# Kernel optimization log

Hardware: AMD Instinct MI355X
Metric: run time of the kernel (lower is better)

## Reference

```python
import jax, jax.numpy as jnp
import numpy as np

N_E = 1024
E_DIM = 256
BETA = 0.25


def setup_inputs() -> dict:
    key = jax.random.key(0)
    k1, k2 = jax.random.split(key)
    z = jax.random.normal(k1, (32, 256, 32, 32), dtype=jnp.float32)
    # codebook init matches nn.Embedding.weight.data.uniform_(-1/n_e, 1/n_e)
    weight = jax.random.uniform(k2, (N_E, E_DIM), minval=-1.0 / N_E, maxval=1.0 / N_E, dtype=jnp.float32)
    return {"z": z, "weight": weight}


def reference(z, weight):
    B, C, H, W = z.shape  # C == E_DIM
    zp = jnp.transpose(z, (0, 2, 3, 1))          # (B,H,W,C)
    zf = zp.reshape(-1, C)                        # (N, e_dim)
    # squared-distance to every codebook entry: ||z||^2 + ||e||^2 - 2 z.e
    d = (jnp.sum(zf * zf, axis=1, keepdims=True)
         + jnp.sum(weight * weight, axis=1)
         - 2.0 * zf @ weight.T)                   # (N, n_e)
    idx = jnp.argmin(d, axis=1)                   # (N,)
    # one-hot @ weight == direct gather (same math, no dense one-hot)
    z_q = weight[idx].reshape(zp.shape)           # (B,H,W,C)
    loss = (jnp.mean((jax.lax.stop_gradient(z_q) - zp) ** 2)
            + BETA * jnp.mean((z_q - jax.lax.stop_gradient(zp)) ** 2))
    # straight-through estimator
    z_q_st = zp + jax.lax.stop_gradient(z_q - zp)
    # codebook usage (mean of one-hot encodings) -> perplexity
    counts = jnp.zeros((N_E,), jnp.float32).at[idx].add(1.0)
    e_mean = counts / zf.shape[0]
    perplexity = jnp.exp(-jnp.sum(e_mean * jnp.log(e_mean + 1e-10)))
    z_q_out = jnp.transpose(z_q_st, (0, 3, 1, 2))  # (B,C,H,W)
    encoding_indices = idx.reshape(B, H, W)
    return (loss, z_q_out, perplexity, encoding_indices)
```

## Files before the change

### kernel.cpp

```cpp
#include <hip/hip_runtime.h>
#include <math.h>

#define ZQ_ELEMS 8388608
#define ZQ_OFF 1
#define PPLX_OFF (1 + ZQ_ELEMS)
#define IDX_OFF  (2 + ZQ_ELEMS)

typedef __attribute__((ext_vector_type(8))) short short8;
typedef __attribute__((ext_vector_type(4))) float f32x4;
typedef __attribute__((ext_vector_type(16))) float f32x16;

#define WS_CANDC 8192
#define WS_FLAG  139264
#define WS_LIST  270336
#define WS_W2    1843200
#define WS_EBF   1847296

static __device__ __forceinline__ ushort f2bf(float f) {
    uint u = __float_as_uint(f);
    return (ushort)((u + 0x7fffu + ((u >> 16) & 1u)) >> 16);
}

__global__ __launch_bounds__(256) void vq_zero(uint* ws) {
    for (int i = blockIdx.x * 256 + threadIdx.x; i < 67584; i += 64 * 256) ws[i] = 0u;
}

__global__ __launch_bounds__(64) void vq_prep_w2(const float* __restrict__ w,
                                                 float* __restrict__ w2) {
    const int j = blockIdx.x * 64 + threadIdx.x;
    const float* wr = w + (size_t)j * 256;
    float s = 0.f;
    for (int k4 = 0; k4 < 64; ++k4) {
        float4 v = *(const float4*)(wr + k4 * 4);
        s = fmaf(v.x, v.x, s); s = fmaf(v.y, v.y, s);
        s = fmaf(v.z, v.z, s); s = fmaf(v.w, v.w, s);
    }
    w2[j] = s;
}

__global__ __launch_bounds__(256) void vq_prep_e(const float* __restrict__ w,
                                                 ushort* __restrict__ ebf_l) {
    const int g = blockIdx.x * 256 + threadIdx.x;
    const int j = g >> 5, o = g & 31;
    const float* src = w + (size_t)j * 256 + o * 8;
    float4 v0 = *(const float4*)src;
    float4 v1 = *(const float4*)(src + 4);
    short8 r;
    r[0] = (short)f2bf(v0.x); r[1] = (short)f2bf(v0.y);
    r[2] = (short)f2bf(v0.z); r[3] = (short)f2bf(v0.w);
    r[4] = (short)f2bf(v1.x); r[5] = (short)f2bf(v1.y);
    r[6] = (short)f2bf(v1.z); r[7] = (short)f2bf(v1.w);
    const size_t dst = (size_t)(j >> 5) * 8192 + (size_t)(o >> 1) * 512
                     + (size_t)((j & 31) + (o & 1) * 32) * 8;
    *(short8*)(ebf_l + dst) = r;
}

__global__ __launch_bounds__(256) void vq_sweep(const float* __restrict__ z,
                                                const ushort* __restrict__ ebf_l,
                                                const float* __restrict__ w2,
                                                uint* __restrict__ candc,
                                                uint* __restrict__ safeflag,
                                                ushort* __restrict__ lists) {
    __shared__ ushort lcl[128][16];
    __shared__ uint lcnt[128];
    __shared__ float sTr[128];

    const int t = threadIdx.x, wv = t >> 6, l = t & 63;
    const int jq = blockIdx.x & 3, rb = blockIdx.x >> 2;
    const int n0 = rb * 128 + wv * 32;
    const int b = n0 >> 10, hw0 = n0 & 1023;
    const int lj = l & 31, hi = l >> 5;

    for (int i = t; i < 128; i += 256) lcnt[i] = 0u;

    const float* zb = z + (size_t)b * 262144 + hw0 + lj;
    short8 as[16];
    float z2p = 0.f;
    #pragma unroll
    for (int s = 0; s < 16; ++s) {
        short8 fr;
        #pragma unroll
        for (int i = 0; i < 8; ++i) {
            const int k = s * 16 + hi * 8 + i;
            float f = zb[(size_t)k << 10];
            z2p = fmaf(f, f, z2p);
            fr[i] = (short)f2bf(f);
        }
        as[s] = fr;
    }
    z2p += __shfl_xor(z2p, 32);
    if (hi == 0) sTr[wv * 32 + lj] = -2.617e-3f * sqrtf(z2p);
    __syncthreads();

    int rloc[16];
    float TrW[16];
    #pragma unroll
    for (int q = 0; q < 16; ++q) {
        rloc[q] = wv * 32 + (q & 3) + 8 * (q >> 2) + 4 * hi;
        TrW[q] = sTr[rloc[q]];
    }

    const int jbase = jq * 256;
    float w2v[8];
    #pragma unroll
    for (int g = 0; g < 8; ++g) w2v[g] = w2[jbase + g * 32 + lj];

    uint safem = 0u;
    for (int g = 0; g < 8; ++g) {
        const ushort* bt = ebf_l + (size_t)(jq * 8 + g) * 8192;
        f32x16 acc = {};
        #pragma unroll
        for (int s = 0; s < 16; ++s) {
            short8 bf = *(const short8*)(bt + s * 512 + l * 8);
            acc = __builtin_amdgcn_mfma_f32_32x32x16_bf16(as[s], bf, acc, 0, 0, 0);
        }
        const int j = jbase + g * 32 + lj;
        float sv[16];
        bool anyhit = false;
        #pragma unroll
        for (int q = 0; q < 16; ++q) {
            sv[q] = fmaf(-2.f, acc[q], w2v[g]);
            anyhit = anyhit || (sv[q] <= TrW[q]);
        }
        if (__any(anyhit)) {
            #pragma unroll
            for (int q = 0; q < 16; ++q)
                if (sv[q] <= TrW[q]) {
                    uint pos = atomicAdd(&lcnt[rloc[q]], 1u);
                    if (pos < 16u) lcl[rloc[q]][pos] = (ushort)j;
                    if (sv[q] <= TrW[q] - 1.5e-3f) safem |= (1u << q);
                }
        }
    }

    #pragma unroll
    for (int off = 1; off < 32; off <<= 1) safem |= __shfl_xor(safem, off);
    if (lj == 0) {
        #pragma unroll
        for (int q = 0; q < 16; ++q)
            if (safem & (1u << q)) safeflag[rb * 128 + rloc[q]] = 1u;
    }
    __syncthreads();

    if (t < 128) {
        const uint lc = lcnt[t];
        const int n = rb * 128 + t;
        if (lc > 16u) atomicAdd(&candc[n], 100u);
        else if (lc) {
            uint base = atomicAdd(&candc[n], lc);
            for (uint i = 0; i < lc && base + i < 24u; ++i)
                lists[(size_t)n * 24 + base + i] = lcl[t][i];
        }
    }
}

__global__ __launch_bounds__(256) void vq_refine(const float* __restrict__ z,
                                                 const float* __restrict__ w,
                                                 const float* __restrict__ w2,
                                                 const uint* __restrict__ candc,
                                                 const uint* __restrict__ safeflag,
                                                 const ushort* __restrict__ lists,
                                                 float* __restrict__ out,
                                                 float* __restrict__ ws) {
    __shared__ float tile[256][64];
    __shared__ float sz2[64];
    __shared__ int sjmin[64];
    __shared__ int scnt[64];
    __shared__ int soff[65];
    __shared__ uint swl[1536];
    __shared__ float sd[1536];
    __shared__ unsigned long long sfbm;
    __shared__ unsigned long long sred[4];
    __shared__ float lred[4];

    const int t = threadIdx.x;
    const int n0 = blockIdx.x * 64;
    const int b = n0 >> 10, hw0 = n0 & 1023;

    if (t == 0) sfbm = 0ull;

    {
        const int r4 = t & 15, cb = t >> 4;
        for (int i = 0; i < 16; ++i) {
            const int c = i * 16 + cb;
            float4 v = *(const float4*)(z + ((size_t)(b * 256 + c) << 10) + hw0 + r4 * 4);
            *(float4*)&tile[c][r4 * 4] = v;
        }
    }
    __syncthreads();

    if (t < 64) {
        float s = 0.f;
        for (int k = 0; k < 256; ++k) { float v = tile[k][t]; s = fmaf(v, v, s); }
        sz2[t] = s;
    }
    if (t < 64) {
        const int n = n0 + t;
        uint c = candc[n];
        bool fb = (safeflag[n] == 0u) || (c == 0u) || (c > 24u);
        scnt[t] = fb ? 0 : (int)c;
        if (fb) atomicOr(&sfbm, 1ull << t);
    }
    __syncthreads();
    if (t == 0) {
        int acc = 0;
        for (int r = 0; r < 64; ++r) { soff[r] = acc; acc += scnt[r]; }
        soff[64] = acc;
    }
    __syncthreads();
    if (t < 64) {
        const int o = soff[t], c = scnt[t], n = n0 + t;
        for (int i = 0; i < c; ++i) swl[o + i] = ((uint)t << 16) | (uint)lists[(size_t)n * 24 + i];
    }
    __syncthreads();

    const int total = soff[64];
    for (int e = t; e < total; e += 256) {
        const int r = (int)(swl[e] >> 16);
        const int j = (int)(swl[e] & 0xffffu);
        const float* wr = w + ((size_t)j << 8);
        float dot = 0.f;
        for (int k4 = 0; k4 < 64; ++k4) {
            float4 v = *(const float4*)(wr + k4 * 4);
            const int k0 = k4 * 4;
            dot = fmaf(v.x, tile[k0 + 0][r], dot);
            dot = fmaf(v.y, tile[k0 + 1][r], dot);
            dot = fmaf(v.z, tile[k0 + 2][r], dot);
            dot = fmaf(v.w, tile[k0 + 3][r], dot);
        }
        const float u = sz2[r] + w2[j];
        sd[e] = u - 2.0f * dot;
    }
    __syncthreads();

    if (t < 64 && scnt[t] > 0) {
        float db = 1e30f; int jb = 0;
        const int o = soff[t], c = scnt[t];
        for (int i = 0; i < c; ++i) {
            float d = sd[o + i];
            int j = (int)(swl[o + i] & 0xffffu);
            if (d < db || (d == db && j < jb)) { db = d; jb = j; }
        }
        sjmin[t] = jb;
    }
    __syncthreads();

    unsigned long long fm = sfbm;
    while (fm) {
        const int r = __ffsll(fm) - 1;
        fm &= fm - 1;
        unsigned long long key = ~0ull;
        for (int jj = 0; jj < 4; ++jj) {
            const int j = t * 4 + jj;
            const float* wr = w + ((size_t)j << 8);
            float dot = 0.f;
            for (int k4 = 0; k4 < 64; ++k4) {
                float4 v = *(const float4*)(wr + k4 * 4);
                const int k0 = k4 * 4;
                dot = fmaf(v.x, tile[k0 + 0][r], dot);
                dot = fmaf(v.y, tile[k0 + 1][r], dot);
                dot = fmaf(v.z, tile[k0 + 2][r], dot);
                dot = fmaf(v.w, tile[k0 + 3][r], dot);
            }
            const float u = sz2[r] + w2[j];
            const float d = u - 2.0f * dot;
            unsigned long long kk = ((unsigned long long)__float_as_uint(d) << 32) | (uint)j;
            if (kk < key) key = kk;
        }
        #pragma unroll
        for (int off = 32; off >= 1; off >>= 1) {
            unsigned long long ok = __shfl_xor(key, off);
            if (ok < key) key = ok;
        }
        if ((t & 63) == 0) sred[t >> 6] = key;
        __syncthreads();
        if (t == 0) {
            unsigned long long kk = sred[0];
            for (int i = 1; i < 4; ++i) if (sred[i] < kk) kk = sred[i];
            sjmin[r] = (int)(kk & 0xffffffffull);
        }
        __syncthreads();
    }
    __syncthreads();

    if (t < 64) {
        const int j = sjmin[t];
        out[IDX_OFF + n0 + t] = (float)j;
        atomicAdd((uint*)ws + 64 + j, 1u);
    }

    float lsum = 0.f;
    {
        const int r = t & 63, cq = t >> 6;
        const float* wrow = w + ((size_t)sjmin[r] << 8);
        for (int i = 0; i < 16; ++i) {
            const int c0 = (i * 4 + cq) * 4;
            float4 v = *(const float4*)(wrow + c0);
            float d0 = v.x - tile[c0 + 0][r];
            float d1 = v.y - tile[c0 + 1][r];
            float d2 = v.z - tile[c0 + 2][r];
            float d3 = v.w - tile[c0 + 3][r];
            lsum += d0 * d0 + d1 * d1 + d2 * d2 + d3 * d3;
            tile[c0 + 0][r] = v.x;
            tile[c0 + 1][r] = v.y;
            tile[c0 + 2][r] = v.z;
            tile[c0 + 3][r] = v.w;
        }
    }
    __syncthreads();

    {
        const int r4 = t & 15, cb = t >> 4;
        for (int i = 0; i < 16; ++i) {
            const int c = i * 16 + cb;
            float4 v = *(const float4*)&tile[c][r4 * 4];
            *(float4*)(out + ZQ_OFF + ((size_t)(b * 256 + c) << 10) + hw0 + r4 * 4) = v;
        }
    }

    for (int off = 32; off >= 1; off >>= 1) lsum += __shfl_xor(lsum, off, 64);
    if ((t & 63) == 0) lred[t >> 6] = lsum;
    __syncthreads();
    if (t == 0) atomicAdd(ws, lred[0] + lred[1] + lred[2] + lred[3]);
}

__global__ __launch_bounds__(1024) void vq_fin(float* __restrict__ out,
                                               float* __restrict__ ws) {
    __shared__ float red[16];
    const int t = threadIdx.x;
    const uint cnt = ((const uint*)ws)[64 + t];
    const float e = (float)cnt * (1.0f / 32768.0f);
    float s = e * logf(e + 1e-10f);
    for (int off = 32; off >= 1; off >>= 1) s += __shfl_xor(s, off, 64);
    if ((t & 63) == 0) red[t >> 6] = s;
    __syncthreads();
    if (t == 0) {
        float H = 0.f;
        for (int i = 0; i < 16; ++i) H += red[i];
        out[PPLX_OFF] = expf(-H);
        const float l = ws[0] * (1.0f / 8388608.0f);
        out[0] = l + 0.25f * l;
    }
}

extern "C" void kernel_launch(void* const* d_in, const int* in_sizes, int n_in,
                              void* d_out, int out_size, void* d_ws, size_t ws_size,
                              hipStream_t stream) {
    const float* z = (const float*)d_in[0];
    const float* w = (const float*)d_in[1];
    float* out = (float*)d_out;
    float* ws = (float*)d_ws;

    uint* candc = (uint*)((char*)d_ws + WS_CANDC);
    uint* safeflag = (uint*)((char*)d_ws + WS_FLAG);
    ushort* lists = (ushort*)((char*)d_ws + WS_LIST);
    float* w2 = (float*)((char*)d_ws + WS_W2);
    ushort* ebf_l = (ushort*)((char*)d_ws + WS_EBF);

    vq_zero<<<64, 256, 0, stream>>>((uint*)d_ws);
    vq_prep_w2<<<16, 64, 0, stream>>>(w, w2);
    vq_prep_e<<<128, 256, 0, stream>>>(w, ebf_l);
    vq_sweep<<<1024, 256, 0, stream>>>(z, ebf_l, w2, candc, safeflag, lists);
    vq_refine<<<512, 256, 0, stream>>>(z, w, w2, candc, safeflag, lists, out, ws);
    vq_fin<<<1, 1024, 0, stream>>>(out, ws);
}
```

Measured before the change: 250.8 us.

## Split refine into argmin and emit kernels; dual MFMA accumulators in sweep

The sweep kernel's inner MFMA chain now alternates between two independent accumulators, which shortens the dependent MFMA chain. The refine kernel is split in two. The argmin stage only computes and stores the indices and histogram counts. A new emit kernel, launched on 1024 blocks of 32 rows, re-reads z, gathers codebook rows, accumulates the loss and writes z_q with scalar stores. This trades an extra launch, a second read of z and a round trip of the indices through float output for lower register and shared-memory pressure and more parallelism in the output stage.

```diff
diff --git a/kernel.cpp b/kernel.cpp
--- a/kernel.cpp
+++ b/kernel.cpp
@@ -109,17 +109,20 @@
     for (int g = 0; g < 8; ++g) {
         const ushort* bt = ebf_l + (size_t)(jq * 8 + g) * 8192;
         f32x16 acc = {};
-        #pragma unroll
-        for (int s = 0; s < 16; ++s) {
-            short8 bf = *(const short8*)(bt + s * 512 + l * 8);
-            acc = __builtin_amdgcn_mfma_f32_32x32x16_bf16(as[s], bf, acc, 0, 0, 0);
+        f32x16 acc2 = {};
+        #pragma unroll
+        for (int s = 0; s < 16; s += 2) {
+            short8 bf  = *(const short8*)(bt + s * 512 + l * 8);
+            short8 bf2 = *(const short8*)(bt + (s + 1) * 512 + l * 8);
+            acc  = __builtin_amdgcn_mfma_f32_32x32x16_bf16(as[s],     bf,  acc,  0, 0, 0);
+            acc2 = __builtin_amdgcn_mfma_f32_32x32x16_bf16(as[s + 1], bf2, acc2, 0, 0, 0);
         }
         const int j = jbase + g * 32 + lj;
         float sv[16];
         bool anyhit = false;
         #pragma unroll
         for (int q = 0; q < 16; ++q) {
-            sv[q] = fmaf(-2.f, acc[q], w2v[g]);
+            sv[q] = fmaf(-2.f, acc[q] + acc2[q], w2v[g]);
             anyhit = anyhit || (sv[q] <= TrW[q]);
         }
         if (__any(anyhit)) {
@@ -154,7 +157,7 @@
     }
 }
 
-__global__ __launch_bounds__(256) void vq_refine(const float* __restrict__ z,
+__global__ __launch_bounds__(256) void vq_argmin(const float* __restrict__ z,
                                                  const float* __restrict__ w,
                                                  const float* __restrict__ w2,
                                                  const uint* __restrict__ candc,
@@ -171,7 +174,6 @@
     __shared__ float sd[1536];
     __shared__ unsigned long long sfbm;
     __shared__ unsigned long long sred[4];
-    __shared__ float lred[4];
 
     const int t = threadIdx.x;
     const int n0 = blockIdx.x * 64;
@@ -288,13 +290,37 @@
         out[IDX_OFF + n0 + t] = (float)j;
         atomicAdd((uint*)ws + 64 + j, 1u);
     }
+}
+
+__global__ __launch_bounds__(256) void vq_emit(const float* __restrict__ z,
+                                               const float* __restrict__ w,
+                                               float* __restrict__ out,
+                                               float* __restrict__ ws) {
+    __shared__ float tile[256][32];
+    __shared__ int sj[32];
+    __shared__ float lred[4];
+
+    const int t = threadIdx.x;
+    const int n0 = blockIdx.x * 32;
+    const int b = n0 >> 10, hw0 = n0 & 1023;
+
+    if (t < 32) sj[t] = (int)out[IDX_OFF + n0 + t];
+    {
+        const int r4 = t & 7, cb = t >> 3;
+        for (int i = 0; i < 8; ++i) {
+            const int c = i * 32 + cb;
+            float4 v = *(const float4*)(z + ((size_t)(b * 256 + c) << 10) + hw0 + r4 * 4);
+            *(float4*)&tile[c][r4 * 4] = v;
+        }
+    }
+    __syncthreads();
 
     float lsum = 0.f;
     {
-        const int r = t & 63, cq = t >> 6;
-        const float* wrow = w + ((size_t)sjmin[r] << 8);
-        for (int i = 0; i < 16; ++i) {
-            const int c0 = (i * 4 + cq) * 4;
+        const int r = t & 31, cq = t >> 5;
+        const float* wrow = w + ((size_t)sj[r] << 8);
+        for (int i = 0; i < 8; ++i) {
+            const int c0 = (i * 8 + cq) * 4;
             float4 v = *(const float4*)(wrow + c0);
             float d0 = v.x - tile[c0 + 0][r];
             float d1 = v.y - tile[c0 + 1][r];
@@ -310,11 +336,10 @@
     __syncthreads();
 
     {
-        const int r4 = t & 15, cb = t >> 4;
-        for (int i = 0; i < 16; ++i) {
-            const int c = i * 16 + cb;
-            float4 v = *(const float4*)&tile[c][r4 * 4];
-            *(float4*)(out + ZQ_OFF + ((size_t)(b * 256 + c) << 10) + hw0 + r4 * 4) = v;
+        const int r = t & 31, ch = (t >> 5) & 1, wv = t >> 6;
+        for (int i = 0; i < 32; ++i) {
+            const int c = i * 8 + wv * 2 + ch;
+            out[ZQ_OFF + ((size_t)(b * 256 + c) << 10) + hw0 + r] = tile[c][r];
         }
     }
 
@@ -361,6 +386,7 @@
     vq_prep_w2<<<16, 64, 0, stream>>>(w, w2);
     vq_prep_e<<<128, 256, 0, stream>>>(w, ebf_l);
     vq_sweep<<<1024, 256, 0, stream>>>(z, ebf_l, w2, candc, safeflag, lists);
-    vq_refine<<<512, 256, 0, stream>>>(z, w, w2, candc, safeflag, lists, out, ws);
+    vq_argmin<<<512, 256, 0, stream>>>(z, w, w2, candc, safeflag, lists, out, ws);
+    vq_emit<<<1024, 256, 0, stream>>>(z, w, out, ws);
     vq_fin<<<1, 1024, 0, stream>>>(out, ws);
 }
```

Result: slower. 276.5 us (+10.3%).
